# Optimization experiments

Hardware: AMD Instinct MI355X
Metric: run time of the kernel (lower is better)

Reference implementation:

```python
import jax, jax.numpy as jnp
import numpy as np

B, S, D = 32, 512, 512
H, DH = 8, 64          # head_num, att_embedding_size
DFF = 4 * D
NEG = float(-2**32 + 1)
LN_EPS = 1e-3          # keras LayerNormalization default


def layer_norm(x, gamma, beta):
    mu = jnp.mean(x, axis=-1, keepdims=True)
    var = jnp.mean(jnp.square(x - mu), axis=-1, keepdims=True)
    return (x - mu) / jnp.sqrt(var + LN_EPS) * gamma + beta


def setup_inputs() -> dict:
    key = jax.random.key(0)
    ks = jax.random.split(key, 10)
    queries = jax.random.normal(ks[0], (B, S, D), dtype=jnp.float32)
    keys = jax.random.normal(ks[1], (B, S, D), dtype=jnp.float32)
    query_lens = jax.random.randint(ks[2], (B, 1), 1, S + 1)
    key_lens = jax.random.randint(ks[3], (B, 1), 1, S + 1)
    # learned params (TruncatedNormal stddev 0.05-ish / Glorot approximated by scaled normals)
    W_Q = jax.random.normal(ks[4], (D, D), dtype=jnp.float32) * 0.05
    W_K = jax.random.normal(ks[5], (D, D), dtype=jnp.float32) * 0.05
    W_V = jax.random.normal(ks[6], (D, D), dtype=jnp.float32) * 0.05
    fw1 = jax.random.normal(ks[7], (D, DFF), dtype=jnp.float32) * (1.0 / np.sqrt(D))
    fw2 = jax.random.normal(ks[8], (DFF, D), dtype=jnp.float32) * (1.0 / np.sqrt(DFF))
    ln_gamma = jnp.ones((D,), dtype=jnp.float32)
    ln_beta = jnp.zeros((D,), dtype=jnp.float32)
    return {"queries": queries, "keys": keys, "W_Q": W_Q, "W_K": W_K, "W_V": W_V,
            "fw1": fw1, "fw2": fw2, "ln_gamma": ln_gamma, "ln_beta": ln_beta,
            "query_lens": query_lens, "key_lens": key_lens}


def reference(queries, keys, W_Q, W_K, W_V, fw1, fw2, ln_gamma, ln_beta, query_lens, key_lens):
    # masks from sequence lengths: [B, S] float {0,1}
    pos = jnp.arange(S)
    q_mask = (pos[None, :] < query_lens).astype(queries.dtype)  # [B,S]
    k_mask = (pos[None, :] < key_lens).astype(queries.dtype)    # [B,S]

    # QKV projections, split into heads: [B,S,H,DH]
    Q = (queries @ W_Q).reshape(B, S, H, DH)
    Kp = (keys @ W_K).reshape(B, S, H, DH)
    V = (keys @ W_V).reshape(B, S, H, DH)

    # scaled dot-product scores: [B,H,Sq,Sk]
    scores = jnp.einsum('bqhd,bkhd->bhqk', Q, Kp) / jnp.sqrt(jnp.asarray(DH, queries.dtype))

    # key padding mask
    scores = jnp.where(k_mask[:, None, None, :] == 1, scores, NEG)
    # blinding: kill the diagonal (self-position)
    eye = jnp.eye(S, dtype=bool)
    scores = jnp.where(eye[None, None, :, :], NEG, scores)

    scores = scores - jnp.max(scores, axis=-1, keepdims=True)
    attn = jax.nn.softmax(scores, axis=-1)
    # query mask zeros out padded query rows (after softmax, as in source)
    attn = attn * q_mask[:, None, :, None]

    out = jnp.einsum('bhqk,bkhd->bqhd', attn, V).reshape(B, S, D)

    result = out + queries                       # use_res
    result = layer_norm(result, ln_gamma, ln_beta)  # shared ln (use_layer_norm)

    # feed-forward
    h = jax.nn.relu(result @ fw1) @ fw2
    result = result + h
    result = layer_norm(result, ln_gamma, ln_beta)

    # output_type == 'mean'
    return jnp.mean(result, axis=1, keepdims=True)  # [B,1,D]
```

## Files before the change

### kernel.cpp

```cpp
#include <hip/hip_runtime.h>

typedef unsigned short ushort_t;
typedef unsigned int uint_t;
typedef __attribute__((ext_vector_type(4))) float f32x4;
typedef __attribute__((ext_vector_type(2))) float f32x2;
typedef __attribute__((ext_vector_type(8))) short s16x8;
typedef __attribute__((ext_vector_type(8))) _Float16 f16x8;
typedef __attribute__((ext_vector_type(4))) unsigned short u16x4;

#define NEGV -60000.0f

__device__ __forceinline__ ushort_t f2bf(float f) {
  unsigned int u = __builtin_bit_cast(unsigned int, f);
  return (ushort_t)((u + 0x7fffu + ((u >> 16) & 1u)) >> 16);
}
__device__ __forceinline__ float bf2f(ushort_t h) {
  unsigned int u = ((unsigned int)h) << 16;
  return __builtin_bit_cast(float, u);
}
__device__ __forceinline__ void gload_lds16(const void* g, void* l) {
  __builtin_amdgcn_global_load_lds(
      (const __attribute__((address_space(1))) unsigned int*)g,
      (__attribute__((address_space(3))) unsigned int*)l, 16, 0, 0);
}

template<int EPI>
__global__ __launch_bounds__(256)
void gemm_bt(const ushort_t* __restrict__ A, const ushort_t* __restrict__ A2,
             int lda,
             const ushort_t* __restrict__ Bt, int ldb,
             void* __restrict__ Cv, int ldc, int K,
             long long sB, long long sC)
{
  __shared__ ushort_t As[3][128 * 32];
  __shared__ ushort_t Bs[3][128 * 32];

  const int tid = threadIdx.x;
  const int w = tid >> 6;
  const int lane = tid & 63;
  const int z = blockIdx.z;

  const ushort_t* Az = (z == 0) ? A : A2;
  const ushort_t* Bz = Bt + (size_t)z * sB;

  const int orig = blockIdx.x + gridDim.x * blockIdx.y;
  const int bx = (orig >> 3) % gridDim.x;
  const int by = (orig & 7) + 8 * ((orig >> 3) / gridDim.x);
  const int m0 = by * 128;
  const int n0 = bx * 128;

  const int wm = (w >> 1) * 64;
  const int wn = (w & 1) * 64;

  f32x4 acc[4][4];
#pragma unroll
  for (int m = 0; m < 4; ++m)
#pragma unroll
    for (int n = 0; n < 4; ++n)
      acc[m][n] = (f32x4){0.f, 0.f, 0.f, 0.f};

  const int cA0 = w * 64 + lane;
  const int cA1 = 256 + cA0;
  const int rA0 = cA0 >> 2, kO0 = (((cA0 & 3) ^ ((rA0 >> 1) & 3)) * 8);
  const int rA1 = cA1 >> 2, kO1 = (((cA1 & 3) ^ ((rA1 >> 1) & 3)) * 8);

  auto stage = [&](int p, int k0) {
    gload_lds16(Az + (size_t)(m0 + rA0) * lda + (k0 + kO0),
                As[p] + (size_t)(w * 64) * 8);
    gload_lds16(Az + (size_t)(m0 + rA1) * lda + (k0 + kO1),
                As[p] + (size_t)(256 + w * 64) * 8);
    gload_lds16(Bz + (size_t)(n0 + rA0) * ldb + (k0 + kO0),
                Bs[p] + (size_t)(w * 64) * 8);
    gload_lds16(Bz + (size_t)(n0 + rA1) * ldb + (k0 + kO1),
                Bs[p] + (size_t)(256 + w * 64) * 8);
  };

  const int nk = K >> 5;
  stage(0, 0);
  stage(1, 32);
  for (int kt = 0; kt < nk; ++kt) {
    const int p = kt % 3;
    if (kt + 2 < nk) {
      stage((kt + 2) % 3, (kt + 2) << 5);
      asm volatile("s_waitcnt vmcnt(8)" ::: "memory");
    } else if (kt + 1 < nk) {
      asm volatile("s_waitcnt vmcnt(4)" ::: "memory");
    } else {
      asm volatile("s_waitcnt vmcnt(0)" ::: "memory");
    }
    __builtin_amdgcn_s_barrier();

    s16x8 af[4], bfr[4];
#pragma unroll
    for (int m = 0; m < 4; ++m) {
      const int r = wm + m * 16 + (lane & 15);
      af[m] = *(const s16x8*)(As[p] + (size_t)r * 32 +
                              (((lane >> 4) ^ ((r >> 1) & 3)) * 8));
    }
#pragma unroll
    for (int n = 0; n < 4; ++n) {
      const int r = wn + n * 16 + (lane & 15);
      bfr[n] = *(const s16x8*)(Bs[p] + (size_t)r * 32 +
                               (((lane >> 4) ^ ((r >> 1) & 3)) * 8));
    }
    __builtin_amdgcn_s_setprio(1);
#pragma unroll
    for (int m = 0; m < 4; ++m)
#pragma unroll
      for (int n = 0; n < 4; ++n)
        acc[m][n] = __builtin_amdgcn_mfma_f32_16x16x32_bf16(af[m], bfr[n],
                                                            acc[m][n], 0, 0, 0);
    __builtin_amdgcn_s_setprio(0);
    __builtin_amdgcn_s_barrier();
  }

  const float s0 = (EPI == 4 && z == 0) ? 0.125f : 1.0f;
  char* Cz = (char*)Cv + (size_t)sC * z;
  const int r_base = (lane >> 4) * 4;
  const int c_base = lane & 15;
#pragma unroll
  for (int m = 0; m < 4; ++m)
#pragma unroll
    for (int n = 0; n < 4; ++n)
#pragma unroll
      for (int j = 0; j < 4; ++j) {
        const int rg = m0 + wm + m * 16 + r_base + j;
        const int cg = n0 + wn + n * 16 + c_base;
        float v = acc[m][n][j];
        const size_t idx = (size_t)rg * ldc + cg;
        if constexpr (EPI == 0) {
          ((float*)Cz)[idx] = v;
        } else if constexpr (EPI == 2) {
          ((ushort_t*)Cz)[idx] = f2bf(fmaxf(v, 0.f));
        } else {
          ((ushort_t*)Cz)[idx] = f2bf(v * s0);
        }
      }
}

__global__ __launch_bounds__(256, 4)
void flash_attn(const ushort_t* __restrict__ Qg, const ushort_t* __restrict__ Kg,
                const ushort_t* __restrict__ Vt, ushort_t* __restrict__ AOb,
                const int* __restrict__ qlen, const int* __restrict__ klen)
{
  __shared__ ushort_t sm[20480];
  ushort_t* PQ = sm + 16384;

  const int tid = threadIdx.x, w = tid >> 6, lane = tid & 63;
  const int fr = lane & 15, fq = lane >> 4;

  int id = blockIdx.x;
  id = (id & 7) * 256 + (id >> 3);
  const int qt = id & 7, h = (id >> 3) & 7, b = id >> 6;
  const int q0 = qt * 64;
  const int KL = klen[b], QL = qlen[b];

  if (q0 >= QL) {
#pragma unroll
    for (int i = 0; i < 4; ++i) {
      int idx = i * 256 + tid;
      int rr = idx >> 4, cc = (idx & 15) << 2;
      *(u16x4*)&AOb[((size_t)(b * 512 + q0 + rr)) * 512 + h * 64 + cc] =
          (u16x4){0, 0, 0, 0};
    }
    return;
  }

  int nt = (KL + 63) >> 6;
  if (KL == 1) nt = 8;

  const ushort_t* Qrow = Qg + ((size_t)(b * 512 + q0)) * 512 + h * 64;
  const ushort_t* Krow = Kg + ((size_t)b * 512) * 512 + h * 64;
  const ushort_t* Vrow = Vt + (((size_t)b * 8 + h) * 64) * 512;

#pragma unroll
  for (int i = 0; i < 2; ++i) {
    int s = i * 256 + tid, r = s >> 3, c = (s & 7) ^ (r & 7);
    gload_lds16(Qrow + (size_t)r * 512 + c * 8, PQ + (i * 256 + w * 64) * 8);
  }
#pragma unroll
  for (int i = 0; i < 2; ++i) {
    int s = i * 256 + tid, r = s >> 3, c = (s & 7) ^ (r & 7);
    gload_lds16(Krow + (size_t)r * 512 + c * 8, sm + (i * 256 + w * 64) * 8);
    gload_lds16(Vrow + (size_t)r * 512 + c * 8, sm + 4096 + (i * 256 + w * 64) * 8);
  }
  __syncthreads();

  s16x8 qf[2];
#pragma unroll
  for (int kc = 0; kc < 2; ++kc) {
    int r = w * 16 + fr;
    qf[kc] = *(const s16x8*)(PQ + r * 64 + (((kc * 4 + fq) ^ (r & 7)) * 8));
  }

  float mrun[4], lrun[4];
  f32x4 oacc[4];
#pragma unroll
  for (int j = 0; j < 4; ++j) { mrun[j] = -1e30f; lrun[j] = 0.f; }
#pragma unroll
  for (int nd = 0; nd < 4; ++nd) oacc[nd] = (f32x4){0.f, 0.f, 0.f, 0.f};

  for (int t = 0; t < nt; ++t) {
    ushort_t* Kb = sm + (t & 1) * 8192;
    ushort_t* Vb = Kb + 4096;
    if (t + 1 < nt) {
      const int kv1 = (t + 1) * 64;
      ushort_t* Kn = sm + ((t + 1) & 1) * 8192;
#pragma unroll
      for (int i = 0; i < 2; ++i) {
        int s = i * 256 + tid, r = s >> 3, c = (s & 7) ^ (r & 7);
        gload_lds16(Krow + (size_t)(kv1 + r) * 512 + c * 8,
                    Kn + (i * 256 + w * 64) * 8);
        gload_lds16(Vrow + (size_t)r * 512 + kv1 + c * 8,
                    Kn + 4096 + (i * 256 + w * 64) * 8);
      }
    }
    const int kv0 = t * 64;

    f32x4 sacc[4];
#pragma unroll
    for (int n = 0; n < 4; ++n) sacc[n] = (f32x4){0.f, 0.f, 0.f, 0.f};
#pragma unroll
    for (int n = 0; n < 4; ++n)
#pragma unroll
      for (int kc = 0; kc < 2; ++kc) {
        int r = n * 16 + fr;
        s16x8 kf = *(const s16x8*)(Kb + r * 64 + (((kc * 4 + fq) ^ (r & 7)) * 8));
        sacc[n] = __builtin_amdgcn_mfma_f32_16x16x32_bf16(qf[kc], kf, sacc[n], 0, 0, 0);
      }

#pragma unroll
    for (int j = 0; j < 4; ++j) {
      const int rl = w * 16 + fq * 4 + j;
      const int rg = q0 + rl;
      float sv[4];
      float tmax = -1e30f;
#pragma unroll
      for (int n = 0; n < 4; ++n) {
        int cg = kv0 + n * 16 + fr;
        float v = sacc[n][j];
        if (cg >= KL || cg == rg) v = NEGV;
        sv[n] = v;
        tmax = fmaxf(tmax, v);
      }
#pragma unroll
      for (int o = 1; o < 16; o <<= 1) tmax = fmaxf(tmax, __shfl_xor(tmax, o));
      const float mnew = fmaxf(mrun[j], tmax);
      const float sf = __expf(mrun[j] - mnew);
      mrun[j] = mnew;
      float ps = 0.f;
      _Float16* prow = (_Float16*)(PQ + rl * 64);
#pragma unroll
      for (int n = 0; n < 4; ++n) {
        float p = __expf(sv[n] - mnew);
        ps += p;
        int cl = n * 2 + (fr >> 3);
        prow[((cl ^ (rl & 7)) * 8) + (fr & 7)] = (_Float16)p;
      }
      lrun[j] = lrun[j] * sf + ps;
#pragma unroll
      for (int nd = 0; nd < 4; ++nd) oacc[nd][j] *= sf;
    }

#pragma unroll
    for (int kc = 0; kc < 2; ++kc) {
      const int rl = w * 16 + fr;
      s16x8 pf = *(const s16x8*)(PQ + rl * 64 + (((kc * 4 + fq) ^ (rl & 7)) * 8));
#pragma unroll
      for (int nd = 0; nd < 4; ++nd) {
        int d = nd * 16 + fr;
        s16x8 vf = *(const s16x8*)(Vb + d * 64 + (((kc * 4 + fq) ^ (d & 7)) * 8));
        oacc[nd] = __builtin_amdgcn_mfma_f32_16x16x32_f16(
            __builtin_bit_cast(f16x8, pf), __builtin_bit_cast(f16x8, vf),
            oacc[nd], 0, 0, 0);
      }
    }
    __syncthreads();
  }

#pragma unroll
  for (int j = 0; j < 4; ++j) {
    float l = lrun[j];
#pragma unroll
    for (int o = 1; o < 16; o <<= 1) l += __shfl_xor(l, o);
    const int rg = q0 + w * 16 + fq * 4 + j;
    const float inv = (rg < QL) ? (1.f / l) : 0.f;
#pragma unroll
    for (int nd = 0; nd < 4; ++nd)
      AOb[((size_t)(b * 512 + rg)) * 512 + h * 64 + nd * 16 + fr] =
          f2bf(oacc[nd][j] * inv);
  }
}

__global__ __launch_bounds__(256) void cvt_bf16(const float* __restrict__ in,
                                                ushort_t* __restrict__ out, int n4) {
  int i = blockIdx.x * 256 + threadIdx.x;
  if (i >= n4) return;
  f32x4 v = ((const f32x4*)in)[i];
  u16x4 o;
#pragma unroll
  for (int j = 0; j < 4; ++j) o[j] = f2bf(v[j]);
  ((u16x4*)out)[i] = o;
}

__global__ __launch_bounds__(256) void transpose_cvt(const float* __restrict__ in,
                                                     ushort_t* __restrict__ out,
                                                     int R, int C) {
  __shared__ float tile[32][33];
  const int c0 = blockIdx.x * 32, r0 = blockIdx.y * 32;
  const int tx = threadIdx.x & 31, ty = threadIdx.x >> 5;
#pragma unroll
  for (int i = 0; i < 32; i += 8)
    tile[ty + i][tx] = in[(size_t)(r0 + ty + i) * C + (c0 + tx)];
  __syncthreads();
#pragma unroll
  for (int i = 0; i < 32; i += 8)
    out[(size_t)(c0 + ty + i) * R + (r0 + tx)] = f2bf(tile[tx][ty + i]);
}

__global__ __launch_bounds__(256) void build_vt(const ushort_t* __restrict__ V,
                                                ushort_t* __restrict__ Vt) {
  __shared__ ushort_t tile[64 * 65];
  const int s0 = blockIdx.x * 64, h = blockIdx.y, b = blockIdx.z;
  const int t = threadIdx.x;
#pragma unroll
  for (int i = 0; i < 16; ++i) {
    int idx = i * 256 + t;
    int sl = idx >> 6, d = idx & 63;
    tile[sl * 65 + d] = V[(size_t)(b * 512 + s0 + sl) * 512 + h * 64 + d];
  }
  __syncthreads();
  _Float16* vt = (_Float16*)Vt;
#pragma unroll
  for (int i = 0; i < 16; ++i) {
    int idx = i * 256 + t;
    int d = idx >> 6, sl = idx & 63;
    vt[((size_t)(b * 8 + h) * 64 + d) * 512 + (s0 + sl)] =
        (_Float16)bf2f(tile[sl * 65 + d]);
  }
}

__global__ __launch_bounds__(256) void ln1(const ushort_t* __restrict__ xb,
                                           const float* __restrict__ r,
                                           const float* __restrict__ g,
                                           const float* __restrict__ be,
                                           ushort_t* __restrict__ ob) {
  const int row = blockIdx.x, t = threadIdx.x;
  const size_t base = (size_t)row * 512;
  const uint_t xv = ((const uint_t*)(xb + base))[t];
  const f32x2 rv = ((const f32x2*)(r + base))[t];
  float v0 = bf2f((ushort_t)(xv & 0xffff)) + rv[0];
  float v1 = bf2f((ushort_t)(xv >> 16)) + rv[1];
  float s = v0 + v1, q = v0 * v0 + v1 * v1;
#pragma unroll
  for (int o = 32; o; o >>= 1) { s += __shfl_xor(s, o); q += __shfl_xor(q, o); }
  __shared__ float ps[4], pq[4];
  const int w = t >> 6, lane = t & 63;
  if (lane == 0) { ps[w] = s; pq[w] = q; }
  __syncthreads();
  s = ps[0] + ps[1] + ps[2] + ps[3];
  q = pq[0] + pq[1] + pq[2] + pq[3];
  const float mu = s * 0.001953125f;
  const float var = q * 0.001953125f - mu * mu;
  const float inv = 1.0f / sqrtf(var + 1e-3f);
  const float y0 = (v0 - mu) * inv * g[2 * t] + be[2 * t];
  const float y1 = (v1 - mu) * inv * g[2 * t + 1] + be[2 * t + 1];
  ((uint_t*)(ob + base))[t] = (uint_t)f2bf(y0) | ((uint_t)f2bf(y1) << 16);
}

__global__ __launch_bounds__(256) void ln2(const float* __restrict__ h2a,
                                           const float* __restrict__ h2b,
                                           const ushort_t* __restrict__ r1b,
                                           const float* __restrict__ g,
                                           const float* __restrict__ be,
                                           ushort_t* __restrict__ ob) {
  const int row = blockIdx.x, t = threadIdx.x;
  const size_t base = (size_t)row * 512;
  const f32x2 a = ((const f32x2*)(h2a + base))[t];
  const f32x2 b = ((const f32x2*)(h2b + base))[t];
  const uint_t rv = ((const uint_t*)(r1b + base))[t];
  float v0 = a[0] + b[0] + bf2f((ushort_t)(rv & 0xffff));
  float v1 = a[1] + b[1] + bf2f((ushort_t)(rv >> 16));
  float s = v0 + v1, q = v0 * v0 + v1 * v1;
#pragma unroll
  for (int o = 32; o; o >>= 1) { s += __shfl_xor(s, o); q += __shfl_xor(q, o); }
  __shared__ float ps[4], pq[4];
  const int w = t >> 6, lane = t & 63;
  if (lane == 0) { ps[w] = s; pq[w] = q; }
  __syncthreads();
  s = ps[0] + ps[1] + ps[2] + ps[3];
  q = pq[0] + pq[1] + pq[2] + pq[3];
  const float mu = s * 0.001953125f;
  const float var = q * 0.001953125f - mu * mu;
  const float inv = 1.0f / sqrtf(var + 1e-3f);
  const float y0 = (v0 - mu) * inv * g[2 * t] + be[2 * t];
  const float y1 = (v1 - mu) * inv * g[2 * t + 1] + be[2 * t + 1];
  ((uint_t*)(ob + base))[t] = (uint_t)f2bf(y0) | ((uint_t)f2bf(y1) << 16);
}

__global__ void mean_partial(const ushort_t* __restrict__ r3,
                             float* __restrict__ part) {
  const int sc = blockIdx.x, b = blockIdx.y, d = threadIdx.x;
  float s = 0.f;
#pragma unroll 4
  for (int i = 0; i < 64; ++i)
    s += bf2f(r3[(size_t)(b * 512 + sc * 64 + i) * 512 + d]);
  part[(size_t)(b * 8 + sc) * 512 + d] = s;
}
__global__ void mean_final(const float* __restrict__ part, float* __restrict__ out) {
  const int b = blockIdx.x, d = threadIdx.x;
  float s = 0.f;
#pragma unroll
  for (int i = 0; i < 8; ++i) s += part[(size_t)(b * 8 + i) * 512 + d];
  out[b * 512 + d] = s * (1.0f / 512.0f);
}

extern "C" void kernel_launch(void* const* d_in, const int* in_sizes, int n_in,
                              void* d_out, int out_size, void* d_ws, size_t ws_size,
                              hipStream_t stream) {
  (void)in_sizes; (void)n_in; (void)out_size; (void)ws_size;
  const float* queries = (const float*)d_in[0];
  const float* keys    = (const float*)d_in[1];
  const float* W_Q = (const float*)d_in[2];
  const float* W_K = (const float*)d_in[3];
  const float* W_V = (const float*)d_in[4];
  const float* fw1 = (const float*)d_in[5];
  const float* fw2 = (const float*)d_in[6];
  const float* ln_g = (const float*)d_in[7];
  const float* ln_b = (const float*)d_in[8];
  const int* qlen = (const int*)d_in[9];
  const int* klen = (const int*)d_in[10];
  float* out = (float*)d_out;

  char* ws = (char*)d_ws;
  const size_t MB = 1048576;
  ushort_t* XQ  = (ushort_t*)(ws + 0 * MB);
  ushort_t* XK  = (ushort_t*)(ws + 16 * MB);
  ushort_t* Qb  = (ushort_t*)(ws + 32 * MB);
  ushort_t* Vb  = (ushort_t*)(ws + 64 * MB);
  ushort_t* VT  = (ushort_t*)(ws + 80 * MB);
  ushort_t* AOb = (ushort_t*)(ws + 96 * MB);
  ushort_t* R1B = (ushort_t*)(ws + 112 * MB);
  ushort_t* H1  = (ushort_t*)(ws + 0 * MB);
  float*    H2  = (float*)(ws + 128 * MB);
  ushort_t* R3B = (ushort_t*)(ws + 192 * MB);
  char*     wsw = ws + 208 * MB;
  ushort_t* WQT  = (ushort_t*)(wsw);
  ushort_t* FW1T = (ushort_t*)(wsw + 3 * 524288);
  ushort_t* FW2T = (ushort_t*)(wsw + 3 * 524288 + 2097152);
  float*    PART = (float*)(wsw + 3 * 524288 + 2 * 2097152);

  cvt_bf16<<<8192, 256, 0, stream>>>(queries, XQ, 2097152);
  cvt_bf16<<<8192, 256, 0, stream>>>(keys, XK, 2097152);
  transpose_cvt<<<dim3(16, 16), 256, 0, stream>>>(W_Q, WQT, 512, 512);
  transpose_cvt<<<dim3(16, 16), 256, 0, stream>>>(W_K, WQT + 262144, 512, 512);
  transpose_cvt<<<dim3(16, 16), 256, 0, stream>>>(W_V, WQT + 524288, 512, 512);
  transpose_cvt<<<dim3(64, 16), 256, 0, stream>>>(fw1, FW1T, 512, 2048);
  transpose_cvt<<<dim3(16, 64), 256, 0, stream>>>(fw2, FW2T, 2048, 512);
  gemm_bt<4><<<dim3(4, 128, 3), 256, 0, stream>>>(
      XQ, XK, 512, WQT, 512, (void*)Qb, 512, 512, 262144, 16 * MB);
  build_vt<<<dim3(8, 8, 32), 256, 0, stream>>>(Vb, VT);
  flash_attn<<<2048, 256, 0, stream>>>(Qb, Qb + 8388608, VT, AOb, qlen, klen);
  ln1<<<16384, 256, 0, stream>>>(AOb, queries, ln_g, ln_b, R1B);
  gemm_bt<2><<<dim3(16, 128, 1), 256, 0, stream>>>(
      R1B, R1B, 512, FW1T, 512, (void*)H1, 2048, 512, 0, 0);
  gemm_bt<0><<<dim3(4, 128, 2), 256, 0, stream>>>(
      H1, H1 + 1024, 2048, FW2T, 2048, (void*)H2, 512, 1024, 1024, 32 * MB);
  ln2<<<16384, 256, 0, stream>>>(H2, H2 + 8388608, R1B, ln_g, ln_b, R3B);
  mean_partial<<<dim3(8, 32), 512, 0, stream>>>(R3B, PART);
  mean_final<<<32, 512, 0, stream>>>(PART, out);
}
```

Baseline: 258.8 us.

## Replace 128x128 GEMM with 256x256 tile, 8-wave ping-pong pipelined kernel

Swaps the 3-stage 128x128x32 GEMM for a 256x256x64 tiled kernel with 8 waves per block, double-buffered LDS and fine-grained interleaving of LDS reads, global-to-LDS prefetch and MFMA phases separated by barriers. Larger tiles raise arithmetic intensity and cut global traffic per FLOP. The aim is to keep the matrix units busy while prefetches are in flight. The risk is fewer blocks on these modest GEMMs (e.g. 384 blocks for QKV, 256 for FFN2), more barriers, and higher register and LDS pressure.

```diff
diff --git a/kernel.cpp b/kernel.cpp
--- a/kernel.cpp
+++ b/kernel.cpp
@@ -25,19 +25,19 @@
 }
 
 template<int EPI>
-__global__ __launch_bounds__(256)
-void gemm_bt(const ushort_t* __restrict__ A, const ushort_t* __restrict__ A2,
+__global__ __launch_bounds__(512, 2)
+void gemm256(const ushort_t* __restrict__ A, const ushort_t* __restrict__ A2,
              int lda,
              const ushort_t* __restrict__ Bt, int ldb,
              void* __restrict__ Cv, int ldc, int K,
              long long sB, long long sC)
 {
-  __shared__ ushort_t As[3][128 * 32];
-  __shared__ ushort_t Bs[3][128 * 32];
-
-  const int tid = threadIdx.x;
-  const int w = tid >> 6;
-  const int lane = tid & 63;
+  __shared__ ushort_t Asm[2][16384];
+  __shared__ ushort_t Bsm[2][16384];
+
+  const int tid = threadIdx.x, wid = tid >> 6, lane = tid & 63;
+  const int wr = wid >> 2, wc = wid & 3;
+  const int fr = lane & 15, fq = lane >> 4;
   const int z = blockIdx.z;
 
   const ushort_t* Az = (z == 0) ? A : A2;
@@ -46,87 +46,227 @@
   const int orig = blockIdx.x + gridDim.x * blockIdx.y;
   const int bx = (orig >> 3) % gridDim.x;
   const int by = (orig & 7) + 8 * ((orig >> 3) / gridDim.x);
-  const int m0 = by * 128;
-  const int n0 = bx * 128;
-
-  const int wm = (w >> 1) * 64;
-  const int wn = (w & 1) * 64;
-
-  f32x4 acc[4][4];
-#pragma unroll
-  for (int m = 0; m < 4; ++m)
+  const int m0 = by * 256, n0 = bx * 256;
+
+  const int rr0 = tid >> 3;
+  const int ks = (((tid & 7) ^ (rr0 & 7)) * 8);
+
+  auto stageA = [&](int p, int kt, int h) {
+    const ushort_t* s = Az + (size_t)(m0 + h * 128 + rr0) * lda + kt * 64 + ks;
+    ushort_t* d = &Asm[p][h * 8192 + tid * 8];
+    gload_lds16(s, d);
+    gload_lds16(s + (size_t)64 * lda, d + 4096);
+  };
+  auto stageB = [&](int p, int kt, int h) {
+    const ushort_t* s = Bz + (size_t)(n0 + h * 128 + rr0) * ldb + kt * 64 + ks;
+    ushort_t* d = &Bsm[p][h * 8192 + tid * 8];
+    gload_lds16(s, d);
+    gload_lds16(s + (size_t)64 * ldb, d + 4096);
+  };
+  auto ldA = [&](int p, int mi, int kc) -> s16x8 {
+    const int R = wr * 128 + mi * 16 + fr;
+    return *(const s16x8*)(&Asm[p][R * 64 + (((kc * 4 + fq) ^ (fr & 7)) * 8)]);
+  };
+  auto ldB = [&](int p, int ni, int kc) -> s16x8 {
+    const int R = wc * 64 + ni * 16 + fr;
+    return *(const s16x8*)(&Bsm[p][R * 64 + (((kc * 4 + fq) ^ (fr & 7)) * 8)]);
+  };
+
+  f32x4 acc[8][4];
+#pragma unroll
+  for (int m = 0; m < 8; ++m)
 #pragma unroll
     for (int n = 0; n < 4; ++n)
       acc[m][n] = (f32x4){0.f, 0.f, 0.f, 0.f};
 
-  const int cA0 = w * 64 + lane;
-  const int cA1 = 256 + cA0;
-  const int rA0 = cA0 >> 2, kO0 = (((cA0 & 3) ^ ((rA0 >> 1) & 3)) * 8);
-  const int rA1 = cA1 >> 2, kO1 = (((cA1 & 3) ^ ((rA1 >> 1) & 3)) * 8);
-
-  auto stage = [&](int p, int k0) {
-    gload_lds16(Az + (size_t)(m0 + rA0) * lda + (k0 + kO0),
-                As[p] + (size_t)(w * 64) * 8);
-    gload_lds16(Az + (size_t)(m0 + rA1) * lda + (k0 + kO1),
-                As[p] + (size_t)(256 + w * 64) * 8);
-    gload_lds16(Bz + (size_t)(n0 + rA0) * ldb + (k0 + kO0),
-                Bs[p] + (size_t)(w * 64) * 8);
-    gload_lds16(Bz + (size_t)(n0 + rA1) * ldb + (k0 + kO1),
-                Bs[p] + (size_t)(256 + w * 64) * 8);
-  };
-
-  const int nk = K >> 5;
-  stage(0, 0);
-  stage(1, 32);
-  for (int kt = 0; kt < nk; ++kt) {
-    const int p = kt % 3;
-    if (kt + 2 < nk) {
-      stage((kt + 2) % 3, (kt + 2) << 5);
-      asm volatile("s_waitcnt vmcnt(8)" ::: "memory");
-    } else if (kt + 1 < nk) {
+  const int nk = K >> 6;
+  const int niter = nk >> 1;
+
+  stageB(0, 0, 0); stageB(0, 0, 1);
+  stageA(0, 0, 0); stageA(0, 0, 1);
+  stageB(1, 1, 0); stageB(1, 1, 1);
+  asm volatile("s_waitcnt vmcnt(4)" ::: "memory");
+  __builtin_amdgcn_s_barrier();
+
+  s16x8 af[4][2], bf[4][2];
+
+  for (int it = 0; it < niter; ++it) {
+    const int T = 2 * it;
+    const bool more = (it + 1 < niter);
+
+#pragma unroll
+    for (int mi = 0; mi < 4; ++mi)
+#pragma unroll
+      for (int kc = 0; kc < 2; ++kc) af[mi][kc] = ldA(0, mi, kc);
+#pragma unroll
+    for (int ni = 0; ni < 2; ++ni)
+#pragma unroll
+      for (int kc = 0; kc < 2; ++kc) bf[ni][kc] = ldB(0, ni, kc);
+    stageA(1, T + 1, 0);
+    __builtin_amdgcn_s_barrier();
+    asm volatile("s_waitcnt lgkmcnt(0)" ::: "memory");
+    __builtin_amdgcn_s_setprio(1);
+#pragma unroll
+    for (int mi = 0; mi < 4; ++mi)
+#pragma unroll
+      for (int ni = 0; ni < 2; ++ni)
+#pragma unroll
+        for (int kc = 0; kc < 2; ++kc)
+          acc[mi][ni] = __builtin_amdgcn_mfma_f32_16x16x32_bf16(
+              af[mi][kc], bf[ni][kc], acc[mi][ni], 0, 0, 0);
+    __builtin_amdgcn_s_setprio(0);
+    __builtin_amdgcn_s_barrier();
+
+#pragma unroll
+    for (int ni = 2; ni < 4; ++ni)
+#pragma unroll
+      for (int kc = 0; kc < 2; ++kc) bf[ni][kc] = ldB(0, ni, kc);
+    stageA(1, T + 1, 1);
+    __builtin_amdgcn_s_barrier();
+    asm volatile("s_waitcnt lgkmcnt(0)" ::: "memory");
+    __builtin_amdgcn_s_setprio(1);
+#pragma unroll
+    for (int mi = 0; mi < 4; ++mi)
+#pragma unroll
+      for (int ni = 2; ni < 4; ++ni)
+#pragma unroll
+        for (int kc = 0; kc < 2; ++kc)
+          acc[mi][ni] = __builtin_amdgcn_mfma_f32_16x16x32_bf16(
+              af[mi][kc], bf[ni][kc], acc[mi][ni], 0, 0, 0);
+    __builtin_amdgcn_s_setprio(0);
+    __builtin_amdgcn_s_barrier();
+
+#pragma unroll
+    for (int mi = 0; mi < 4; ++mi)
+#pragma unroll
+      for (int kc = 0; kc < 2; ++kc) af[mi][kc] = ldA(0, 4 + mi, kc);
+    if (more) stageB(0, T + 2, 0);
+    __builtin_amdgcn_s_barrier();
+    asm volatile("s_waitcnt lgkmcnt(0)" ::: "memory");
+    __builtin_amdgcn_s_setprio(1);
+#pragma unroll
+    for (int mi = 0; mi < 4; ++mi)
+#pragma unroll
+      for (int ni = 0; ni < 2; ++ni)
+#pragma unroll
+        for (int kc = 0; kc < 2; ++kc)
+          acc[4 + mi][ni] = __builtin_amdgcn_mfma_f32_16x16x32_bf16(
+              af[mi][kc], bf[ni][kc], acc[4 + mi][ni], 0, 0, 0);
+    __builtin_amdgcn_s_setprio(0);
+    __builtin_amdgcn_s_barrier();
+
+    if (more) {
+      stageB(0, T + 2, 1);
       asm volatile("s_waitcnt vmcnt(4)" ::: "memory");
     } else {
       asm volatile("s_waitcnt vmcnt(0)" ::: "memory");
     }
     __builtin_amdgcn_s_barrier();
-
-    s16x8 af[4], bfr[4];
-#pragma unroll
-    for (int m = 0; m < 4; ++m) {
-      const int r = wm + m * 16 + (lane & 15);
-      af[m] = *(const s16x8*)(As[p] + (size_t)r * 32 +
-                              (((lane >> 4) ^ ((r >> 1) & 3)) * 8));
+    __builtin_amdgcn_s_setprio(1);
+#pragma unroll
+    for (int mi = 0; mi < 4; ++mi)
+#pragma unroll
+      for (int ni = 2; ni < 4; ++ni)
+#pragma unroll
+        for (int kc = 0; kc < 2; ++kc)
+          acc[4 + mi][ni] = __builtin_amdgcn_mfma_f32_16x16x32_bf16(
+              af[mi][kc], bf[ni][kc], acc[4 + mi][ni], 0, 0, 0);
+    __builtin_amdgcn_s_setprio(0);
+    __builtin_amdgcn_s_barrier();
+
+#pragma unroll
+    for (int mi = 0; mi < 4; ++mi)
+#pragma unroll
+      for (int kc = 0; kc < 2; ++kc) af[mi][kc] = ldA(1, mi, kc);
+#pragma unroll
+    for (int ni = 0; ni < 2; ++ni)
+#pragma unroll
+      for (int kc = 0; kc < 2; ++kc) bf[ni][kc] = ldB(1, ni, kc);
+    if (more) stageA(0, T + 2, 0);
+    __builtin_amdgcn_s_barrier();
+    asm volatile("s_waitcnt lgkmcnt(0)" ::: "memory");
+    __builtin_amdgcn_s_setprio(1);
+#pragma unroll
+    for (int mi = 0; mi < 4; ++mi)
+#pragma unroll
+      for (int ni = 0; ni < 2; ++ni)
+#pragma unroll
+        for (int kc = 0; kc < 2; ++kc)
+          acc[mi][ni] = __builtin_amdgcn_mfma_f32_16x16x32_bf16(
+              af[mi][kc], bf[ni][kc], acc[mi][ni], 0, 0, 0);
+    __builtin_amdgcn_s_setprio(0);
+    __builtin_amdgcn_s_barrier();
+
+#pragma unroll
+    for (int ni = 2; ni < 4; ++ni)
+#pragma unroll
+      for (int kc = 0; kc < 2; ++kc) bf[ni][kc] = ldB(1, ni, kc);
+    if (more) stageA(0, T + 2, 1);
+    __builtin_amdgcn_s_barrier();
+    asm volatile("s_waitcnt lgkmcnt(0)" ::: "memory");
+    __builtin_amdgcn_s_setprio(1);
+#pragma unroll
+    for (int mi = 0; mi < 4; ++mi)
+#pragma unroll
+      for (int ni = 2; ni < 4; ++ni)
+#pragma unroll
+        for (int kc = 0; kc < 2; ++kc)
+          acc[mi][ni] = __builtin_amdgcn_mfma_f32_16x16x32_bf16(
+              af[mi][kc], bf[ni][kc], acc[mi][ni], 0, 0, 0);
+    __builtin_amdgcn_s_setprio(0);
+    __builtin_amdgcn_s_barrier();
+
+#pragma unroll
+    for (int mi = 0; mi < 4; ++mi)
+#pragma unroll
+      for (int kc = 0; kc < 2; ++kc) af[mi][kc] = ldA(1, 4 + mi, kc);
+    if (more) stageB(1, T + 3, 0);
+    __builtin_amdgcn_s_barrier();
+    asm volatile("s_waitcnt lgkmcnt(0)" ::: "memory");
+    __builtin_amdgcn_s_setprio(1);
+#pragma unroll
+    for (int mi = 0; mi < 4; ++mi)
+#pragma unroll
+      for (int ni = 0; ni < 2; ++ni)
+#pragma unroll
+        for (int kc = 0; kc < 2; ++kc)
+          acc[4 + mi][ni] = __builtin_amdgcn_mfma_f32_16x16x32_bf16(
+              af[mi][kc], bf[ni][kc], acc[4 + mi][ni], 0, 0, 0);
+    __builtin_amdgcn_s_setprio(0);
+    __builtin_amdgcn_s_barrier();
+
+    if (more) {
+      stageB(1, T + 3, 1);
+      asm volatile("s_waitcnt vmcnt(4)" ::: "memory");
+    } else {
+      asm volatile("s_waitcnt vmcnt(0)" ::: "memory");
     }
-#pragma unroll
-    for (int n = 0; n < 4; ++n) {
-      const int r = wn + n * 16 + (lane & 15);
-      bfr[n] = *(const s16x8*)(Bs[p] + (size_t)r * 32 +
-                               (((lane >> 4) ^ ((r >> 1) & 3)) * 8));
-    }
-    __builtin_amdgcn_s_setprio(1);
-#pragma unroll
-    for (int m = 0; m < 4; ++m)
-#pragma unroll
-      for (int n = 0; n < 4; ++n)
-        acc[m][n] = __builtin_amdgcn_mfma_f32_16x16x32_bf16(af[m], bfr[n],
-                                                            acc[m][n], 0, 0, 0);
+    __builtin_amdgcn_s_barrier();
+    __builtin_amdgcn_s_setprio(1);
+#pragma unroll
+    for (int mi = 0; mi < 4; ++mi)
+#pragma unroll
+      for (int ni = 2; ni < 4; ++ni)
+#pragma unroll
+        for (int kc = 0; kc < 2; ++kc)
+          acc[4 + mi][ni] = __builtin_amdgcn_mfma_f32_16x16x32_bf16(
+              af[mi][kc], bf[ni][kc], acc[4 + mi][ni], 0, 0, 0);
     __builtin_amdgcn_s_setprio(0);
     __builtin_amdgcn_s_barrier();
   }
 
   const float s0 = (EPI == 4 && z == 0) ? 0.125f : 1.0f;
   char* Cz = (char*)Cv + (size_t)sC * z;
-  const int r_base = (lane >> 4) * 4;
-  const int c_base = lane & 15;
-#pragma unroll
-  for (int m = 0; m < 4; ++m)
-#pragma unroll
-    for (int n = 0; n < 4; ++n)
+  const int rb = fq * 4;
+#pragma unroll
+  for (int mi = 0; mi < 8; ++mi)
+#pragma unroll
+    for (int ni = 0; ni < 4; ++ni)
 #pragma unroll
       for (int j = 0; j < 4; ++j) {
-        const int rg = m0 + wm + m * 16 + r_base + j;
-        const int cg = n0 + wn + n * 16 + c_base;
-        float v = acc[m][n][j];
+        const int rg = m0 + wr * 128 + mi * 16 + rb + j;
+        const int cg = n0 + wc * 64 + ni * 16 + fr;
+        float v = acc[mi][ni][j];
         const size_t idx = (size_t)rg * ldc + cg;
         if constexpr (EPI == 0) {
           ((float*)Cz)[idx] = v;
@@ -457,14 +597,14 @@
   transpose_cvt<<<dim3(16, 16), 256, 0, stream>>>(W_V, WQT + 524288, 512, 512);
   transpose_cvt<<<dim3(64, 16), 256, 0, stream>>>(fw1, FW1T, 512, 2048);
   transpose_cvt<<<dim3(16, 64), 256, 0, stream>>>(fw2, FW2T, 2048, 512);
-  gemm_bt<4><<<dim3(4, 128, 3), 256, 0, stream>>>(
+  gemm256<4><<<dim3(2, 64, 3), 512, 0, stream>>>(
       XQ, XK, 512, WQT, 512, (void*)Qb, 512, 512, 262144, 16 * MB);
   build_vt<<<dim3(8, 8, 32), 256, 0, stream>>>(Vb, VT);
   flash_attn<<<2048, 256, 0, stream>>>(Qb, Qb + 8388608, VT, AOb, qlen, klen);
   ln1<<<16384, 256, 0, stream>>>(AOb, queries, ln_g, ln_b, R1B);
-  gemm_bt<2><<<dim3(16, 128, 1), 256, 0, stream>>>(
+  gemm256<2><<<dim3(8, 64, 1), 512, 0, stream>>>(
       R1B, R1B, 512, FW1T, 512, (void*)H1, 2048, 512, 0, 0);
-  gemm_bt<0><<<dim3(4, 128, 2), 256, 0, stream>>>(
+  gemm256<0><<<dim3(2, 64, 2), 512, 0, stream>>>(
       H1, H1 + 1024, 2048, FW2T, 2048, (void*)H2, 512, 1024, 1024, 32 * MB);
   ln2<<<16384, 256, 0, stream>>>(H2, H2 + 8388608, R1B, ln_g, ln_b, R3B);
   mean_partial<<<dim3(8, 32), 512, 0, stream>>>(R3B, PART);
```

After: 247.3 us. 1.05x faster.
